# Optimization experiments

Measured on AMD Instinct MI355X. Metric: run time of the kernel, lower is better.

The kernel has to match this reference:

```python
import jax, jax.numpy as jnp
import numpy as np

NUM_ROUTERS = 8
K = 2
IN_DIM = 384
HID = 64
TEMP = 1.0
AUX_COEF = 0.05
EPS = 1e-12


def _l2norm(v, axis=-1):
    n = jnp.sqrt(jnp.sum(v * v, axis=axis, keepdims=True))
    return v / jnp.maximum(n, EPS)


def setup_inputs() -> dict:
    key = jax.random.key(0)
    ks = jax.random.split(key, 10)
    B, E = 8192, 1024
    s = 1.0 / np.sqrt(IN_DIM)
    return {
        "x": jax.random.normal(ks[0], (B, IN_DIM), jnp.float32),
        "reasoning_embeddings": jax.random.normal(ks[1], (E, IN_DIM), jnp.float32),
        "random_num": jax.random.uniform(ks[2], (B, 1), jnp.float32),
        "gate_w": jax.random.normal(ks[3], (IN_DIM, NUM_ROUTERS), jnp.float32) * s,
        "gate_b": jnp.zeros((NUM_ROUTERS,), jnp.float32),
        "Uw": jax.random.normal(ks[4], (NUM_ROUTERS, IN_DIM, HID), jnp.float32) * s,
        "Ub": jnp.zeros((NUM_ROUTERS, HID), jnp.float32),
        "Vw": jax.random.normal(ks[5], (NUM_ROUTERS, IN_DIM, HID), jnp.float32) * s,
        "Vb": jnp.zeros((NUM_ROUTERS, HID), jnp.float32),
    }


def reference(x, reasoning_embeddings, random_num, gate_w, gate_b, Uw, Ub, Vw, Vb):
    B = x.shape[0]
    # gate
    logits = x @ gate_w + gate_b                              # [B, R]
    probs = jax.nn.softmax(logits, axis=-1)
    topk_vals, topk_idxs = jax.lax.top_k(logits, K)           # [B, K]
    topk_mask = jax.nn.one_hot(topk_idxs, NUM_ROUTERS).sum(axis=1)  # [B, R]
    aux_loss = NUM_ROUTERS * (probs.mean(0) * topk_mask.mean(0)).sum() * AUX_COEF

    # all routers, batched (replaces the per-(i,j) python loop)
    xu = _l2norm(jnp.einsum("bd,rdh->rbh", x, Uw) + Ub[:, None, :])          # [R, B, H]
    ev = _l2norm(jnp.einsum("ed,rdh->reh", reasoning_embeddings, Vw) + Vb[:, None, :])  # [R, E, H]
    scores = jnp.einsum("rbh,reh->rbe", xu, ev)               # [R, B, E]
    all_out = jax.nn.softmax(scores / TEMP, axis=-1)          # [R, B, E]

    # gather top-k experts per sample
    all_out_b = jnp.transpose(all_out, (1, 0, 2))             # [B, R, E]
    router_outputs = jnp.take_along_axis(all_out_b, topk_idxs[:, :, None], axis=1)  # [B, K, E]

    gate_weights = jax.nn.softmax(topk_vals, axis=-1)[:, :, None]  # [B, K, 1]
    rea_probs = jnp.sum(router_outputs * gate_weights, axis=1)     # [B, E]

    # categorical sampling via inverse-CDF
    scores_cumsum = jnp.cumsum(rea_probs, axis=1)
    selected_index = jnp.argmax((scores_cumsum > random_num).astype(jnp.float32), axis=1)  # [B]
    log_probs = jnp.log(rea_probs[jnp.arange(B), selected_index])[:, None]  # [B, 1]
    return selected_index, log_probs, aux_loss
```

## Files before the change

### kernel.cpp

```cpp
#include <hip/hip_runtime.h>
#include <math.h>

#define B 8192
#define E 1024
#define D 384
#define H 64
#define R 8
#define NCHUNK 16
#define CHUNK_E 64
#define NPOS 17408

#define WS_CNT    0u
#define WS_CUR    32u
#define WS_PS     64u
#define WS_OFFS   96u
#define WS_TOP2   256u
#define WS_GW     65792u
#define WS_POSM   131328u
#define WS_LIST   196864u
#define WS_EVN    266496u
#define WS_XUN    2363648u
#define WS_C      6820096u

__global__ __launch_bounds__(256) void k_gate(
    const float* __restrict__ x, const float* __restrict__ gate_w,
    const float* __restrict__ gate_b, int2* __restrict__ top2,
    float2* __restrict__ gwv, int* __restrict__ counts, float* __restrict__ ps)
{
  __shared__ __align__(16) float gwT[R * 388];
  __shared__ float psl[R];
  __shared__ int   cl[R];
  int tid = threadIdx.x;
  for (int idx = tid; idx < D * R; idx += 256) {
    int k = idx >> 3, r = idx & 7;
    gwT[r * 388 + k] = gate_w[idx];
  }
  if (tid < R) { psl[tid] = 0.f; cl[tid] = 0; }
  __syncthreads();

  int l = tid & 63;
  int r = tid & 7;
  int b = blockIdx.x * 32 + (tid >> 3);
  float acc = gate_b[r];
  const float4* x4 = (const float4*)(x + (size_t)b * D);
  const float*  gr = gwT + r * 388;
#pragma unroll 4
  for (int q = 0; q < 96; ++q) {
    float4 xv = x4[q];
    float4 gv = *(const float4*)&gr[q * 4];
    acc = fmaf(xv.x, gv.x, acc);
    acc = fmaf(xv.y, gv.y, acc);
    acc = fmaf(xv.z, gv.z, acc);
    acc = fmaf(xv.w, gv.w, acc);
  }
  float lv[R];
#pragma unroll
  for (int rr = 0; rr < R; ++rr) lv[rr] = __shfl(acc, (l & ~7) + rr);
  int i0 = 0; float v0 = lv[0];
#pragma unroll
  for (int rr = 1; rr < R; ++rr) if (lv[rr] > v0) { v0 = lv[rr]; i0 = rr; }
  int i1 = (i0 == 0) ? 1 : 0; float v1 = lv[i1];
#pragma unroll
  for (int rr = 0; rr < R; ++rr)
    if (rr != i0 && lv[rr] > v1) { v1 = lv[rr]; i1 = rr; }
  float se = 0.f;
#pragma unroll
  for (int rr = 0; rr < R; ++rr) se += expf(lv[rr] - v0);
  float p = expf(acc - v0) / se;
  if (r == 0) {
    float e10 = expf(v1 - v0);
    top2[b] = make_int2(i0, i1);
    gwv[b]  = make_float2(1.f / (1.f + e10), e10 / (1.f + e10));
  }
  float pa = p;
  int   ca = (r == i0 ? 1 : 0) + (r == i1 ? 1 : 0);
#pragma unroll
  for (int m = 8; m < 64; m <<= 1) {
    pa += __shfl_xor(pa, m);
    ca += __shfl_xor(ca, m);
  }
  if (l < 8) { atomicAdd(&psl[r], pa); atomicAdd(&cl[r], ca); }
  __syncthreads();
  if (tid < R) { atomicAdd(&ps[tid], psl[tid]); atomicAdd(&counts[tid], cl[tid]); }
}

__global__ __launch_bounds__(256) void k_scatter(
    const int2* __restrict__ top2, const int* __restrict__ counts,
    const float* __restrict__ ps, int* __restrict__ cursors,
    int* __restrict__ list, int2* __restrict__ posmap,
    int* __restrict__ offs_g, float* __restrict__ out_aux)
{
  __shared__ int lc[R];
  __shared__ int lbase[R];
  __shared__ int offs[R];
  int tid = threadIdx.x;
  if (tid < R) lc[tid] = 0;
  __syncthreads();
  if (tid == 0) {
    int o = 0;
    for (int r2 = 0; r2 < R; ++r2) { offs[r2] = o; o += (min(counts[r2], B) + 127) & ~127; }
  }
  __syncthreads();
  int b = min(blockIdx.x * 256 + tid, B - 1);
  int2 t = top2[b];
  t.x &= 7; t.y &= 7;
  int p0 = atomicAdd(&lc[t.x], 1);
  int p1 = atomicAdd(&lc[t.y], 1);
  __syncthreads();
  if (tid < R) lbase[tid] = atomicAdd(&cursors[tid], lc[tid]);
  __syncthreads();
  int i0 = min(offs[t.x] + lbase[t.x] + p0, NPOS - 1);
  int i1 = min(offs[t.y] + lbase[t.y] + p1, NPOS - 1);
  list[i0] = b * 2 + 0;
  list[i1] = b * 2 + 1;
  posmap[b] = make_int2(i0, i1);
  if (blockIdx.x == 0 && tid == 0) {
    float s = 0.f;
    for (int r2 = 0; r2 < R; ++r2) {
      s += (ps[r2] / (float)B) * ((float)min(counts[r2], B) / (float)B);
      offs_g[r2] = offs[r2];
    }
    out_aux[0] = (float)R * s * 0.05f;
  }
}

__global__ __launch_bounds__(128) void k_projgemm(
    const float* __restrict__ re, const float* __restrict__ x,
    const float* __restrict__ Vw, const float* __restrict__ Uw,
    const float* __restrict__ Vb, const float* __restrict__ Ub,
    const int* __restrict__ list, const int* __restrict__ counts,
    const int* __restrict__ offs, float* __restrict__ evnC,
    float* __restrict__ xunP)
{
  __shared__ __align__(16) float At[2][64 * 64];
  __shared__ __align__(16) float Wt[2][64 * 64];
  int tid = threadIdx.x;
  int tile = blockIdx.x;
  int rowg0 = tile * 64;

  int srow = tid & 63, kh = tid >> 6;
  const float* Wsrc;
  const float* arow;
  int r = 0;
  bool isE = (tile < 128);
  if (isE) {
    r = rowg0 >> 10;
    Wsrc = Vw + (size_t)r * (D * H);
    arow = re + (size_t)((rowg0 & 1023) + srow) * D;
  } else {
    int pos0 = rowg0 - 8192;
    int tot = offs[R - 1] + ((min(counts[R - 1], B) + 127) & ~127);
    if (pos0 >= tot) return;
    for (int rr = 0; rr < R; ++rr) if (pos0 >= offs[rr]) r = rr;
    Wsrc = Uw + (size_t)r * (D * H);
    int gl = list[min(pos0 + srow, NPOS - 1)];
    gl = min(max(gl, 0), 2 * B - 1);
    arow = x + (size_t)(gl >> 1) * D;
  }
  const float4* arow4 = (const float4*)arow;
  const float4* Wsrc4 = (const float4*)Wsrc;

  int rg = tid >> 4, cg = tid & 15;
  float acc[8][4];
#pragma unroll
  for (int i = 0; i < 8; ++i)
#pragma unroll
    for (int j = 0; j < 4; ++j) acc[i][j] = 0.f;

  float4 va[8], vw[8];

#pragma unroll
  for (int q = 0; q < 8; ++q)
    va[q] = arow4[kh * 8 + q];
#pragma unroll
  for (int q = 0; q < 8; ++q) {
    int idx = tid + 128 * q;
    int k = idx >> 4, h4 = idx & 15;
    vw[q] = Wsrc4[(size_t)k * 16 + h4];
  }
#pragma unroll
  for (int q = 0; q < 8; ++q) {
    int k0 = kh * 32 + q * 4;
    At[0][(k0 + 0) * 64 + srow] = va[q].x;
    At[0][(k0 + 1) * 64 + srow] = va[q].y;
    At[0][(k0 + 2) * 64 + srow] = va[q].z;
    At[0][(k0 + 3) * 64 + srow] = va[q].w;
  }
#pragma unroll
  for (int q = 0; q < 8; ++q) {
    int idx = tid + 128 * q;
    int k = idx >> 4, h4 = idx & 15;
    *(float4*)&Wt[0][k * 64 + h4 * 4] = vw[q];
  }
  __syncthreads();

  for (int kt = 0; kt < 6; ++kt) {
    int cur = kt & 1;
    if (kt < 5) {
      int kb4 = (kt + 1) * 16;
#pragma unroll
      for (int q = 0; q < 8; ++q)
        va[q] = arow4[kb4 + kh * 8 + q];
#pragma unroll
      for (int q = 0; q < 8; ++q) {
        int idx = tid + 128 * q;
        int k = idx >> 4, h4 = idx & 15;
        vw[q] = Wsrc4[(size_t)((kt + 1) * 64 + k) * 16 + h4];
      }
    }
    {
      const float4* At4 = (const float4*)&At[cur][0];
      const float4* Wt4 = (const float4*)&Wt[cur][0];
#pragma unroll 8
      for (int k = 0; k < 64; ++k) {
        float4 a0 = At4[(k * 64 + rg * 8) >> 2];
        float4 a1 = At4[(k * 64 + rg * 8 + 4) >> 2];
        float4 w4 = Wt4[(k * 64 + cg * 4) >> 2];
        const float* a0p = (const float*)&a0;
        const float* a1p = (const float*)&a1;
        const float* wp  = (const float*)&w4;
#pragma unroll
        for (int i = 0; i < 4; ++i)
#pragma unroll
          for (int j = 0; j < 4; ++j) {
            acc[i][j]     = fmaf(a0p[i], wp[j], acc[i][j]);
            acc[i + 4][j] = fmaf(a1p[i], wp[j], acc[i + 4][j]);
          }
      }
    }
    if (kt < 5) {
      int nxt = cur ^ 1;
#pragma unroll
      for (int q = 0; q < 8; ++q) {
        int k0 = kh * 32 + q * 4;
        At[nxt][(k0 + 0) * 64 + srow] = va[q].x;
        At[nxt][(k0 + 1) * 64 + srow] = va[q].y;
        At[nxt][(k0 + 2) * 64 + srow] = va[q].z;
        At[nxt][(k0 + 3) * 64 + srow] = va[q].w;
      }
#pragma unroll
      for (int q = 0; q < 8; ++q) {
        int idx = tid + 128 * q;
        int k = idx >> 4, h4 = idx & 15;
        *(float4*)&Wt[nxt][k * 64 + h4 * 4] = vw[q];
      }
    }
    __syncthreads();
  }

  const float* bsrc = (isE ? Vb : Ub) + r * H + cg * 4;
  float4 bv = *(const float4*)bsrc;
#pragma unroll
  for (int i = 0; i < 8; ++i) {
    acc[i][0] += bv.x;
    acc[i][1] += bv.y;
    acc[i][2] += bv.z;
    acc[i][3] += bv.w;
    float ss = acc[i][0] * acc[i][0] + acc[i][1] * acc[i][1]
             + acc[i][2] * acc[i][2] + acc[i][3] * acc[i][3];
#pragma unroll
    for (int m = 1; m < 16; m <<= 1) ss += __shfl_xor(ss, m);
    float dn = fmaxf(sqrtf(ss), 1e-12f);
    acc[i][0] /= dn; acc[i][1] /= dn; acc[i][2] /= dn; acc[i][3] /= dn;
  }

  if (!isE) {
    int pos0 = rowg0 - 8192;
#pragma unroll
    for (int i = 0; i < 8; ++i) {
      float4 o;
      o.x = acc[i][0]; o.y = acc[i][1]; o.z = acc[i][2]; o.w = acc[i][3];
      *(float4*)&xunP[(size_t)(pos0 + rg * 8 + i) * H + cg * 4] = o;
    }
    return;
  }

  float* scratch = &At[0][0];
  int cidx = (rowg0 & 1023) >> 6;
#pragma unroll
  for (int i = 0; i < 8; ++i)
#pragma unroll
    for (int j = 0; j < 4; ++j)
      scratch[(cg * 4 + j) * 66 + rg * 8 + i] = acc[i][j];
  __syncthreads();
  float* dst = evnC + (size_t)(r * NCHUNK + cidx) * 64 * 64;
#pragma unroll
  for (int q = 0; q < 8; ++q) {
    int idx = tid + 128 * q;
    int h = idx >> 4, f4 = idx & 15;
    float4 o;
    o.x = scratch[h * 66 + f4 * 4 + 0];
    o.y = scratch[h * 66 + f4 * 4 + 1];
    o.z = scratch[h * 66 + f4 * 4 + 2];
    o.w = scratch[h * 66 + f4 * 4 + 3];
    *(float4*)&dst[h * 64 + f4 * 4] = o;
  }
}

__global__ __launch_bounds__(256) void k_pass1(
    const float* __restrict__ evnC, const float* __restrict__ xunP,
    const int* __restrict__ counts, const int* __restrict__ offs,
    float* __restrict__ C)
{
  __shared__ __align__(16) float Xt[32 * 128];
  __shared__ __align__(16) float Et[32 * 128];
  int tid = threadIdx.x;
  int bid = blockIdx.x;
  int et    = bid & 7;
  int stile = (bid >> 3) & 63;
  int r     = bid >> 9;
  int cnt = min(counts[r], B);
  if (cnt <= 0 || stile * 128 >= cnt) return;
  int off = offs[r] + stile * 128;
  int n = min(128, cnt - stile * 128);

  int sg = tid >> 4, egr = tid & 15;
  float acc[8][8];
#pragma unroll
  for (int i = 0; i < 8; ++i)
#pragma unroll
    for (int j = 0; j < 8; ++j) acc[i][j] = 0.f;

  int srow = tid >> 1, shalf = tid & 1;
  int src = min(srow, n - 1);
  const float4* xsrc = (const float4*)(xunP + (size_t)(off + src) * H);

  float4 xv[4], ev[4];
#pragma unroll
  for (int q = 0; q < 4; ++q) xv[q] = xsrc[shalf * 4 + q];
#pragma unroll
  for (int q = 0; q < 4; ++q) {
    int idx = tid + 256 * q;
    int h = idx >> 5, e4 = idx & 31;
    int cc = et * 2 + (e4 >> 4);
    ev[q] = *(const float4*)(evnC + ((size_t)(r * NCHUNK + cc) * 64 + h) * 64
                             + (e4 & 15) * 4);
  }
#pragma unroll
  for (int q = 0; q < 4; ++q) {
    int hb = shalf * 16 + q * 4;
    Xt[(hb + 0) * 128 + srow] = xv[q].x;
    Xt[(hb + 1) * 128 + srow] = xv[q].y;
    Xt[(hb + 2) * 128 + srow] = xv[q].z;
    Xt[(hb + 3) * 128 + srow] = xv[q].w;
  }
#pragma unroll
  for (int q = 0; q < 4; ++q) {
    int idx = tid + 256 * q;
    int h = idx >> 5, e4 = idx & 31;
    *(float4*)&Et[h * 128 + e4 * 4] = ev[q];
  }
#pragma unroll
  for (int q = 0; q < 4; ++q) xv[q] = xsrc[8 + shalf * 4 + q];
#pragma unroll
  for (int q = 0; q < 4; ++q) {
    int idx = tid + 256 * q;
    int h = idx >> 5, e4 = idx & 31;
    int cc = et * 2 + (e4 >> 4);
    ev[q] = *(const float4*)(evnC + ((size_t)(r * NCHUNK + cc) * 64 + 32 + h) * 64
                             + (e4 & 15) * 4);
  }
  __syncthreads();

  auto compute32 = [&]() {
#pragma unroll 4
    for (int k = 0; k < 32; ++k) {
      float4 xa = *(const float4*)&Xt[k * 128 + sg * 4];
      float4 xb = *(const float4*)&Xt[k * 128 + 64 + sg * 4];
      float4 ea = *(const float4*)&Et[k * 128 + egr * 4];
      float4 eb = *(const float4*)&Et[k * 128 + 64 + egr * 4];
      const float* pa = (const float*)&xa;
      const float* pb = (const float*)&xb;
      const float* qa = (const float*)&ea;
      const float* qb = (const float*)&eb;
#pragma unroll
      for (int i = 0; i < 4; ++i)
#pragma unroll
        for (int j = 0; j < 4; ++j) {
          acc[i][j]         = fmaf(pa[i], qa[j], acc[i][j]);
          acc[i][j + 4]     = fmaf(pa[i], qb[j], acc[i][j + 4]);
          acc[i + 4][j]     = fmaf(pb[i], qa[j], acc[i + 4][j]);
          acc[i + 4][j + 4] = fmaf(pb[i], qb[j], acc[i + 4][j + 4]);
        }
    }
  };

  compute32();
  __syncthreads();
#pragma unroll
  for (int q = 0; q < 4; ++q) {
    int hb = shalf * 16 + q * 4;
    Xt[(hb + 0) * 128 + srow] = xv[q].x;
    Xt[(hb + 1) * 128 + srow] = xv[q].y;
    Xt[(hb + 2) * 128 + srow] = xv[q].z;
    Xt[(hb + 3) * 128 + srow] = xv[q].w;
  }
#pragma unroll
  for (int q = 0; q < 4; ++q) {
    int idx = tid + 256 * q;
    int h = idx >> 5, e4 = idx & 31;
    *(float4*)&Et[h * 128 + e4 * 4] = ev[q];
  }
  __syncthreads();
  compute32();

#pragma unroll
  for (int i = 0; i < 8; ++i) {
    float cA = __expf(acc[i][0]) + __expf(acc[i][1]) + __expf(acc[i][2]) + __expf(acc[i][3]);
    float cB = __expf(acc[i][4]) + __expf(acc[i][5]) + __expf(acc[i][6]) + __expf(acc[i][7]);
#pragma unroll
    for (int m = 1; m < 16; m <<= 1) {
      cA += __shfl_xor(cA, m);
      cB += __shfl_xor(cB, m);
    }
    int s = (i < 4) ? (sg * 4 + i) : (64 + sg * 4 + i - 4);
    if (egr == 0 && s < n) {
      C[(size_t)(off + s) * NCHUNK + et * 2]     = cA;
      C[(size_t)(off + s) * NCHUNK + et * 2 + 1] = cB;
    }
  }
}

__global__ __launch_bounds__(256) void k_pass2(
    const float* __restrict__ evnC, const float* __restrict__ xunP,
    const float* __restrict__ C, const int2* __restrict__ top2,
    const int2* __restrict__ posmap, const float2* __restrict__ gwv,
    const float* __restrict__ rnd, float* __restrict__ out)
{
  __shared__ __align__(16) float sxu[4][2][64];
  int tid = threadIdx.x;
  int lane = tid & 63;
  int w = tid >> 6;
  int b = blockIdx.x * 4 + w;
  int2 t2 = top2[b];
  t2.x &= 7; t2.y &= 7;
  int2 pm = posmap[b];
  pm.x = min(max(pm.x, 0), NPOS - 1);
  pm.y = min(max(pm.y, 0), NPOS - 1);
  float2 gw = gwv[b];
  float rv = rnd[b];

  sxu[w][0][lane] = xunP[(size_t)pm.x * H + lane];
  sxu[w][1][lane] = xunP[(size_t)pm.y * H + lane];

  const float4* C04 = (const float4*)(C + (size_t)pm.x * NCHUNK);
  const float4* C14 = (const float4*)(C + (size_t)pm.y * NCHUNK);
  float c0[NCHUNK], c1[NCHUNK];
#pragma unroll
  for (int q = 0; q < 4; ++q) {
    float4 v0 = C04[q], v1 = C14[q];
    c0[q*4+0]=v0.x; c0[q*4+1]=v0.y; c0[q*4+2]=v0.z; c0[q*4+3]=v0.w;
    c1[q*4+0]=v1.x; c1[q*4+1]=v1.y; c1[q*4+2]=v1.z; c1[q*4+3]=v1.w;
  }
  float S0 = 0.f, S1 = 0.f;
#pragma unroll
  for (int j = 0; j < NCHUNK; ++j) { S0 += c0[j]; S1 += c1[j]; }
  float a0 = gw.x / S0, a1 = gw.y / S1;
  int cstar = -1; float prefix = 0.f; float run = 0.f;
#pragma unroll
  for (int j = 0; j < NCHUNK; ++j) {
    float nrun = run + (c0[j] * a0 + c1[j] * a1);
    if (cstar < 0 && nrun > rv) { cstar = j; prefix = run; }
    run = nrun;
  }
  float rtgt = rv;
  if (cstar < 0) { cstar = 0; prefix = 0.f; rtgt = -1.0f; }

  __syncthreads();

  const float4* E0 = (const float4*)(evnC + (size_t)(t2.x * NCHUNK + cstar) * 64 * 64);
  const float4* E1 = (const float4*)(evnC + (size_t)(t2.y * NCHUNK + cstar) * 64 * 64);
  const float* x0 = &sxu[w][0][0];
  const float* x1 = &sxu[w][1][0];
  int hq = lane >> 4;
  float d0[4] = {0.f, 0.f, 0.f, 0.f};
  float d1[4] = {0.f, 0.f, 0.f, 0.f};
#pragma unroll
  for (int q = 0; q < 16; ++q) {
    float4 e0 = E0[q * 64 + lane];
    float4 e1 = E1[q * 64 + lane];
    float w0 = x0[q * 4 + hq];
    float w1 = x1[q * 4 + hq];
    d0[0] = fmaf(e0.x, w0, d0[0]); d0[1] = fmaf(e0.y, w0, d0[1]);
    d0[2] = fmaf(e0.z, w0, d0[2]); d0[3] = fmaf(e0.w, w0, d0[3]);
    d1[0] = fmaf(e1.x, w1, d1[0]); d1[1] = fmaf(e1.y, w1, d1[1]);
    d1[2] = fmaf(e1.z, w1, d1[2]); d1[3] = fmaf(e1.w, w1, d1[3]);
  }
#pragma unroll
  for (int j = 0; j < 4; ++j) {
    d0[j] += __shfl_xor(d0[j], 16);
    d0[j] += __shfl_xor(d0[j], 32);
    d1[j] += __shfl_xor(d1[j], 16);
    d1[j] += __shfl_xor(d1[j], 32);
  }
  float rea[4], inc[4];
  float trun = 0.f;
#pragma unroll
  for (int j = 0; j < 4; ++j) {
    rea[j] = __expf(d0[j]) * a0 + __expf(d1[j]) * a1;
    trun += rea[j];
    inc[j] = trun;
  }
  float sc = trun;
#pragma unroll
  for (int d = 1; d < 16; d <<= 1) {
    float o = __shfl_up(sc, d, 16);
    if ((lane & 15) >= d) sc += o;
  }
  float base = prefix + (sc - trun);
  unsigned long long m2 = __ballot(base + inc[3] > rtgt) & 0xFFFFull;
  int lstar = (m2 == 0ull) ? 15 : (int)__builtin_ctzll(m2);
  int jloc = 3;
  if (base + inc[2] > rtgt) jloc = 2;
  if (base + inc[1] > rtgt) jloc = 1;
  if (base + inc[0] > rtgt) jloc = 0;
  float pl = (jloc == 0) ? rea[0] : (jloc == 1) ? rea[1] : (jloc == 2) ? rea[2] : rea[3];
  int   js = __shfl(jloc, lstar);
  float p  = __shfl(pl, lstar);
  if (lane == 0) {
    int sel = cstar * CHUNK_E + lstar * 4 + js;
    out[b]     = (float)sel;
    out[B + b] = logf(p);
  }
}

extern "C" void kernel_launch(void* const* d_in, const int* in_sizes, int n_in,
                              void* d_out, int out_size, void* d_ws, size_t ws_size,
                              hipStream_t stream)
{
  (void)in_sizes; (void)n_in; (void)out_size; (void)ws_size;
  const float* x      = (const float*)d_in[0];
  const float* re     = (const float*)d_in[1];
  const float* rnd    = (const float*)d_in[2];
  const float* gate_w = (const float*)d_in[3];
  const float* gate_b = (const float*)d_in[4];
  const float* Uw     = (const float*)d_in[5];
  const float* Ub     = (const float*)d_in[6];
  const float* Vw     = (const float*)d_in[7];
  const float* Vb     = (const float*)d_in[8];
  char* ws = (char*)d_ws;
  int*    counts  = (int*)(ws + WS_CNT);
  int*    cursors = (int*)(ws + WS_CUR);
  float*  ps      = (float*)(ws + WS_PS);
  int*    offs    = (int*)(ws + WS_OFFS);
  int2*   top2    = (int2*)(ws + WS_TOP2);
  float2* gwv     = (float2*)(ws + WS_GW);
  int2*   posmap  = (int2*)(ws + WS_POSM);
  int*    list    = (int*)(ws + WS_LIST);
  float*  evnC    = (float*)(ws + WS_EVN);
  float*  xunP    = (float*)(ws + WS_XUN);
  float*  Cc      = (float*)(ws + WS_C);
  float* out = (float*)d_out;

  hipMemsetAsync(ws, 0, 128, stream);
  k_gate    <<<256,  256, 0, stream>>>(x, gate_w, gate_b, top2, gwv, counts, ps);
  k_scatter <<<32,   256, 0, stream>>>(top2, counts, ps, cursors, list, posmap, offs, out + 2 * B);
  k_projgemm<<<400,  128, 0, stream>>>(re, x, Vw, Uw, Vb, Ub, list, counts, offs, evnC, xunP);
  k_pass1   <<<4096, 256, 0, stream>>>(evnC, xunP, counts, offs, Cc);
  k_pass2   <<<2048, 256, 0, stream>>>(evnC, xunP, Cc, top2, posmap, gwv, rnd, out);
}
```

Before: 171.2 us.

## Halve pass1 block to 128 threads with 16x8 register tile per thread

```diff
diff --git a/kernel.cpp b/kernel.cpp
--- a/kernel.cpp
+++ b/kernel.cpp
@@ -297,7 +297,7 @@
   }
 }
 
-__global__ __launch_bounds__(256) void k_pass1(
+__global__ __launch_bounds__(128, 2) void k_pass1(
     const float* __restrict__ evnC, const float* __restrict__ xunP,
     const int* __restrict__ counts, const int* __restrict__ offs,
     float* __restrict__ C)
@@ -315,97 +315,72 @@
   int n = min(128, cnt - stile * 128);
 
   int sg = tid >> 4, egr = tid & 15;
-  float acc[8][8];
-#pragma unroll
-  for (int i = 0; i < 8; ++i)
+  float acc[16][8];
+#pragma unroll
+  for (int i = 0; i < 16; ++i)
 #pragma unroll
     for (int j = 0; j < 8; ++j) acc[i][j] = 0.f;
 
-  int srow = tid >> 1, shalf = tid & 1;
-  int src = min(srow, n - 1);
+  int src = min(tid, n - 1);
   const float4* xsrc = (const float4*)(xunP + (size_t)(off + src) * H);
 
-  float4 xv[4], ev[4];
-#pragma unroll
-  for (int q = 0; q < 4; ++q) xv[q] = xsrc[shalf * 4 + q];
-#pragma unroll
-  for (int q = 0; q < 4; ++q) {
-    int idx = tid + 256 * q;
-    int h = idx >> 5, e4 = idx & 31;
-    int cc = et * 2 + (e4 >> 4);
-    ev[q] = *(const float4*)(evnC + ((size_t)(r * NCHUNK + cc) * 64 + h) * 64
+  for (int kst = 0; kst < 2; ++kst) {
+    if (kst) __syncthreads();
+    {
+#pragma unroll
+      for (int q = 0; q < 8; ++q) {
+        float4 v = xsrc[kst * 8 + q];
+        int hb = q * 4;
+        Xt[(hb + 0) * 128 + tid] = v.x;
+        Xt[(hb + 1) * 128 + tid] = v.y;
+        Xt[(hb + 2) * 128 + tid] = v.z;
+        Xt[(hb + 3) * 128 + tid] = v.w;
+      }
+    }
+    {
+#pragma unroll
+      for (int q = 0; q < 8; ++q) {
+        int idx = tid + 128 * q;
+        int h = idx >> 5, e4 = idx & 31;
+        int cc = et * 2 + (e4 >> 4);
+        *(float4*)&Et[h * 128 + e4 * 4] =
+            *(const float4*)(evnC + ((size_t)(r * NCHUNK + cc) * 64 + kst * 32 + h) * 64
                              + (e4 & 15) * 4);
-  }
-#pragma unroll
-  for (int q = 0; q < 4; ++q) {
-    int hb = shalf * 16 + q * 4;
-    Xt[(hb + 0) * 128 + srow] = xv[q].x;
-    Xt[(hb + 1) * 128 + srow] = xv[q].y;
-    Xt[(hb + 2) * 128 + srow] = xv[q].z;
-    Xt[(hb + 3) * 128 + srow] = xv[q].w;
-  }
-#pragma unroll
-  for (int q = 0; q < 4; ++q) {
-    int idx = tid + 256 * q;
-    int h = idx >> 5, e4 = idx & 31;
-    *(float4*)&Et[h * 128 + e4 * 4] = ev[q];
-  }
-#pragma unroll
-  for (int q = 0; q < 4; ++q) xv[q] = xsrc[8 + shalf * 4 + q];
-#pragma unroll
-  for (int q = 0; q < 4; ++q) {
-    int idx = tid + 256 * q;
-    int h = idx >> 5, e4 = idx & 31;
-    int cc = et * 2 + (e4 >> 4);
-    ev[q] = *(const float4*)(evnC + ((size_t)(r * NCHUNK + cc) * 64 + 32 + h) * 64
-                             + (e4 & 15) * 4);
-  }
-  __syncthreads();
-
-  auto compute32 = [&]() {
-#pragma unroll 4
+      }
+    }
+    __syncthreads();
+#pragma unroll 2
     for (int k = 0; k < 32; ++k) {
-      float4 xa = *(const float4*)&Xt[k * 128 + sg * 4];
-      float4 xb = *(const float4*)&Xt[k * 128 + 64 + sg * 4];
-      float4 ea = *(const float4*)&Et[k * 128 + egr * 4];
-      float4 eb = *(const float4*)&Et[k * 128 + 64 + egr * 4];
-      const float* pa = (const float*)&xa;
-      const float* pb = (const float*)&xb;
-      const float* qa = (const float*)&ea;
-      const float* qb = (const float*)&eb;
-#pragma unroll
-      for (int i = 0; i < 4; ++i)
+      float4 xg0 = *(const float4*)&Xt[k * 128 + sg * 4];
+      float4 xg1 = *(const float4*)&Xt[k * 128 + 32 + sg * 4];
+      float4 xg2 = *(const float4*)&Xt[k * 128 + 64 + sg * 4];
+      float4 xg3 = *(const float4*)&Xt[k * 128 + 96 + sg * 4];
+      float4 ea  = *(const float4*)&Et[k * 128 + egr * 4];
+      float4 eb  = *(const float4*)&Et[k * 128 + 64 + egr * 4];
+      const float* ep = (const float*)&ea;
+      const float* fp = (const float*)&eb;
+      const float* x0p = (const float*)&xg0;
+      const float* x1p = (const float*)&xg1;
+      const float* x2p = (const float*)&xg2;
+      const float* x3p = (const float*)&xg3;
+#pragma unroll
+      for (int i2 = 0; i2 < 4; ++i2)
 #pragma unroll
         for (int j = 0; j < 4; ++j) {
-          acc[i][j]         = fmaf(pa[i], qa[j], acc[i][j]);
-          acc[i][j + 4]     = fmaf(pa[i], qb[j], acc[i][j + 4]);
-          acc[i + 4][j]     = fmaf(pb[i], qa[j], acc[i + 4][j]);
-          acc[i + 4][j + 4] = fmaf(pb[i], qb[j], acc[i + 4][j + 4]);
+          acc[i2][j]          = fmaf(x0p[i2], ep[j], acc[i2][j]);
+          acc[i2][j + 4]      = fmaf(x0p[i2], fp[j], acc[i2][j + 4]);
+          acc[4 + i2][j]      = fmaf(x1p[i2], ep[j], acc[4 + i2][j]);
+          acc[4 + i2][j + 4]  = fmaf(x1p[i2], fp[j], acc[4 + i2][j + 4]);
+          acc[8 + i2][j]      = fmaf(x2p[i2], ep[j], acc[8 + i2][j]);
+          acc[8 + i2][j + 4]  = fmaf(x2p[i2], fp[j], acc[8 + i2][j + 4]);
+          acc[12 + i2][j]     = fmaf(x3p[i2], ep[j], acc[12 + i2][j]);
+          acc[12 + i2][j + 4] = fmaf(x3p[i2], fp[j], acc[12 + i2][j + 4]);
         }
     }
-  };
-
-  compute32();
-  __syncthreads();
-#pragma unroll
-  for (int q = 0; q < 4; ++q) {
-    int hb = shalf * 16 + q * 4;
-    Xt[(hb + 0) * 128 + srow] = xv[q].x;
-    Xt[(hb + 1) * 128 + srow] = xv[q].y;
-    Xt[(hb + 2) * 128 + srow] = xv[q].z;
-    Xt[(hb + 3) * 128 + srow] = xv[q].w;
-  }
-#pragma unroll
-  for (int q = 0; q < 4; ++q) {
-    int idx = tid + 256 * q;
-    int h = idx >> 5, e4 = idx & 31;
-    *(float4*)&Et[h * 128 + e4 * 4] = ev[q];
-  }
-  __syncthreads();
-  compute32();
-
-#pragma unroll
-  for (int i = 0; i < 8; ++i) {
+  }
+
+#pragma unroll
+  for (int i = 0; i < 16; ++i) {
     float cA = __expf(acc[i][0]) + __expf(acc[i][1]) + __expf(acc[i][2]) + __expf(acc[i][3]);
     float cB = __expf(acc[i][4]) + __expf(acc[i][5]) + __expf(acc[i][6]) + __expf(acc[i][7]);
 #pragma unroll
@@ -413,7 +388,7 @@
       cA += __shfl_xor(cA, m);
       cB += __shfl_xor(cB, m);
     }
-    int s = (i < 4) ? (sg * 4 + i) : (64 + sg * 4 + i - 4);
+    int s = (i >> 2) * 32 + sg * 4 + (i & 3);
     if (egr == 0 && s < n) {
       C[(size_t)(off + s) * NCHUNK + et * 2]     = cA;
       C[(size_t)(off + s) * NCHUNK + et * 2 + 1] = cB;
@@ -556,6 +531,6 @@
   k_gate    <<<256,  256, 0, stream>>>(x, gate_w, gate_b, top2, gwv, counts, ps);
   k_scatter <<<32,   256, 0, stream>>>(top2, counts, ps, cursors, list, posmap, offs, out + 2 * B);
   k_projgemm<<<400,  128, 0, stream>>>(re, x, Vw, Uw, Vb, Ub, list, counts, offs, evnC, xunP);
-  k_pass1   <<<4096, 256, 0, stream>>>(evnC, xunP, counts, offs, Cc);
+  k_pass1   <<<4096, 128, 0, stream>>>(evnC, xunP, counts, offs, Cc);
   k_pass2   <<<2048, 256, 0, stream>>>(evnC, xunP, Cc, top2, posmap, gwv, rnd, out);
 }
```

After: 173.9 us. About the same (+1.6%).
